# Optimization experiments

Hardware: AMD Instinct MI355X
Metric: run time of the kernel (lower is better)

The kernel has to match this reference:

```python
import jax, jax.numpy as jnp
from jax import lax
import numpy as np

B, GRID, H = 128, 28, 64      # batch, 28x28 pixel grid, hidden size
NDIR = 4                      # feature_sz = number of scan directions
FC_HD, OUT = 512, 10


def setup_inputs() -> dict:
    key = jax.random.key(0)
    ks = jax.random.split(key, 8)
    s_u = 1.0 / np.sqrt(2 * H)
    inp = {
        "x":  jax.random.normal(ks[0], (B, GRID, GRID), dtype=jnp.float32),
        # per-direction MDLSTM gate params: 5 gates (i, f_left, f_up, o, g)
        "Wx": jax.random.normal(ks[1], (NDIR, 5 * H), dtype=jnp.float32) * 0.1,
        "U":  jax.random.normal(ks[2], (NDIR, 2 * H, 5 * H), dtype=jnp.float32) * s_u,
        "b":  jnp.zeros((NDIR, 5 * H), dtype=jnp.float32),
        # fc head
        "W1": jax.random.normal(ks[3], (NDIR * H, FC_HD), dtype=jnp.float32) / np.sqrt(NDIR * H),
        "b1": jnp.zeros((FC_HD,), dtype=jnp.float32),
        "W2": jax.random.normal(ks[4], (FC_HD, OUT), dtype=jnp.float32) / np.sqrt(FC_HD),
        "b2": jnp.zeros((OUT,), dtype=jnp.float32),
    }
    return inp


def _mdlstm_dir(xg, Wx, U, b):
    # xg: [GRID(rows), GRID(cols), B] scalar pixel per cell
    zeros = jnp.zeros((xg.shape[-1], H), dtype=xg.dtype)

    def col_step(carry, inp):
        h_left, c_left = carry
        x_pix, h_up, c_up = inp                     # [B], [B,H], [B,H]
        z = x_pix[:, None] * Wx + jnp.concatenate([h_left, h_up], -1) @ U + b
        i, f1, f2, o, g = jnp.split(z, 5, axis=-1)  # each [B,H]
        c = (jax.nn.sigmoid(i) * jnp.tanh(g)
             + jax.nn.sigmoid(f1) * c_left
             + jax.nn.sigmoid(f2) * c_up)
        h = jax.nn.sigmoid(o) * jnp.tanh(c)
        return (h, c), (h, c)

    def row_step(carry, x_row):
        h_up_row, c_up_row = carry                  # [GRID,B,H] previous row
        _, (h_row, c_row) = lax.scan(col_step, (zeros, zeros),
                                     (x_row, h_up_row, c_up_row))
        return (h_row, c_row), None

    init = (jnp.zeros((GRID,) + zeros.shape, xg.dtype),
            jnp.zeros((GRID,) + zeros.shape, xg.dtype))
    (h_last_row, _), _ = lax.scan(row_step, init, xg)
    return h_last_row[-1]                           # final (bottom-right) hidden [B,H]


def _forward(x, Wx, U, b, W1, b1, W2, b2):
    x2 = x.reshape(-1, GRID, GRID)
    # 4 scan directions via flips; scan always proceeds top-left -> bottom-right
    dirs = jnp.stack([x2,
                      x2[:, :, ::-1],
                      x2[:, ::-1, :],
                      x2[:, ::-1, ::-1]], 0)        # [4,B,GRID,GRID]
    dirs = jnp.transpose(dirs, (0, 2, 3, 1))        # [4,GRID,GRID,B]
    h = jax.vmap(_mdlstm_dir)(dirs, Wx, U, b)       # [4,B,H]
    h = jnp.transpose(h, (1, 0, 2)).reshape(-1, NDIR * H)
    z = jax.nn.relu(h @ W1 + b1)
    return jax.nn.softmax(z @ W2 + b2, axis=-1)


def reference(x, Wx, U, b, W1, b1, W2, b2):
    return _forward(x, Wx, U, b, W1, b1, W2, b2)
```

## Files before the change

kernel.cpp:

```cpp
#include <hip/hip_runtime.h>
#include <hip/hip_bf16.h>


#define GRIDN 28
#define BATCH 128
#define HID   64
#define NDIR  4
#define FC_HD 512
#define OUT_N 10
#define BT    2
#define NSLOT 29
#define S_H   104
#define S_C   68

typedef _Float16 f16;
typedef _Float16 f16x8 __attribute__((ext_vector_type(8)));
typedef float    f32x4 __attribute__((ext_vector_type(4)));

__device__ __forceinline__ float sigf(float x) {
    return __builtin_amdgcn_rcpf(1.0f + __expf(-x));
}
__device__ __forceinline__ float tanh_fast(float x) {
    return 1.0f - 2.0f * __builtin_amdgcn_rcpf(1.0f + __expf(2.0f * x));
}

__global__ __launch_bounds__(512)
void mdlstm_kernel(const float* __restrict__ x,
                   const float* __restrict__ Wx,
                   const float* __restrict__ U,
                   const float* __restrict__ bias,
                   float* __restrict__ Hout)
{
    const int d    = blockIdx.x & 3;
    const int tile = blockIdx.x >> 2;
    const int tid  = threadIdx.x;
    const int lane = tid & 63;
    const int wave = tid >> 6;
    const int wm   = wave >> 2;
    const int wh   = wave & 3;
    const int l16  = lane & 15;
    const int q    = lane >> 4;
    const int nb   = wh * 16 + l16;

    __shared__ __align__(16) f16 Fh[2][BT][NSLOT * S_H];
    __shared__ float             Fc[2][BT][NSLOT * S_C];
    __shared__ float             xs[GRIDN][GRIDN][BT];

    for (int i = tid; i < 2 * BT * NSLOT * S_H; i += 512) ((f16*)Fh)[i] = (f16)0.0f;
    for (int i = tid; i < 2 * BT * NSLOT * S_C; i += 512) ((float*)Fc)[i] = 0.0f;
    for (int i = tid; i < GRIDN * GRIDN * BT; i += 512) {
        int bl = i & 1, rc = i >> 1, c = rc % GRIDN, r = rc / GRIDN;
        int rr = (d & 2) ? (GRIDN - 1 - r) : r;
        int cc = (d & 1) ? (GRIDN - 1 - c) : c;
        xs[r][c][bl] = x[((tile * BT + bl) * GRIDN + rr) * GRIDN + cc];
    }

    f16x8 bf[5][5];
#pragma unroll
    for (int g = 0; g < 5; ++g) {
        int n = g * 64 + nb;
#pragma unroll
        for (int ks = 0; ks < 4; ++ks) {
            f16x8 v;
            int kb = ks * 32 + q * 8;
#pragma unroll
            for (int j = 0; j < 8; ++j)
                v[j] = (f16)U[(d * 128 + kb + j) * 320 + n];
            bf[g][ks] = v;
        }
        f16x8 v5 = {(f16)0, (f16)0, (f16)0, (f16)0, (f16)0, (f16)0, (f16)0, (f16)0};
        if (q == 0) {
            v5[0] = (f16)Wx[d * 320 + n];
            v5[1] = (f16)bias[d * 320 + n];
        }
        bf[g][4] = v5;
    }
    __syncthreads();

    if (tid < 2 * BT * NSLOT) {
        int buf = tid / (BT * NSLOT), rem = tid % (BT * NSLOT);
        int b = rem / NSLOT, sl = rem % NSLOT;
        Fh[buf][b][sl * S_H + 65] = (f16)1.0f;
    }
    if (tid < BT) Fh[0][tid][27 * S_H + 64] = (f16)xs[0][0][tid];
    __syncthreads();

    for (int t = 0; t < 2 * GRIDN - 1; ++t) {
        const int rlo = (t > GRIDN - 1) ? (t - (GRIDN - 1)) : 0;
        const int rhi = (t < GRIDN - 1) ? t : (GRIDN - 1);
        const int k   = rhi - rlo + 1;
        const int nM  = (2 * k + 15) >> 4;
        const int br  = t & 1, bw = br ^ 1;

        if (t < 2 * GRIDN - 2 && tid >= 456) {
            int idx = tid - 456, b = idx & 1, j = idx >> 1;
            int rlo2 = (t + 1 > GRIDN - 1) ? (t + 1 - (GRIDN - 1)) : 0;
            int rhi2 = (t + 1 < GRIDN - 1) ? (t + 1) : (GRIDN - 1);
            if (j <= rhi2 - rlo2) {
                int r = rlo2 + j;
                Fh[bw][b][(27 - r) * S_H + 64] = (f16)xs[r][t + 1 - r][b];
            }
        }

        for (int mt = wm; mt < nM; mt += 2) {
            int mA = mt * 16 + l16;
            int jA = mA >> 1; if (jA > k - 1) jA = k - 1;
            int bA = mA & 1;
            int slA = 27 - (rlo + jA);
            const f16* ab = &Fh[br][bA][slA * S_H];
            f16x8 a0 = *(const f16x8*)(ab + q * 8);
            f16x8 a1 = *(const f16x8*)(ab + 32 + q * 8);
            f16x8 a2 = *(const f16x8*)(ab + S_H + q * 8);
            f16x8 a3 = *(const f16x8*)(ab + S_H + 32 + q * 8);
            f16x8 a4 = *(const f16x8*)(ab + 64 + q * 8);

            f32x4 acc[5];
#pragma unroll
            for (int g = 0; g < 5; ++g) acc[g] = (f32x4){0.f, 0.f, 0.f, 0.f};
#pragma unroll
            for (int g = 0; g < 5; ++g) acc[g] = __builtin_amdgcn_mfma_f32_16x16x32_f16(a0, bf[g][0], acc[g], 0, 0, 0);
#pragma unroll
            for (int g = 0; g < 5; ++g) acc[g] = __builtin_amdgcn_mfma_f32_16x16x32_f16(a1, bf[g][1], acc[g], 0, 0, 0);
#pragma unroll
            for (int g = 0; g < 5; ++g) acc[g] = __builtin_amdgcn_mfma_f32_16x16x32_f16(a2, bf[g][2], acc[g], 0, 0, 0);
#pragma unroll
            for (int g = 0; g < 5; ++g) acc[g] = __builtin_amdgcn_mfma_f32_16x16x32_f16(a3, bf[g][3], acc[g], 0, 0, 0);
#pragma unroll
            for (int g = 0; g < 5; ++g) acc[g] = __builtin_amdgcn_mfma_f32_16x16x32_f16(a4, bf[g][4], acc[g], 0, 0, 0);

            int j0  = mt * 8 + q * 2;
            int jj0 = (j0     > k - 1) ? k - 1 : j0;
            int jj1 = (j0 + 1 > k - 1) ? k - 1 : j0 + 1;
            int sl0 = 27 - (rlo + jj0);
            int sl1 = 27 - (rlo + jj1);
#pragma unroll
            for (int i = 0; i < 4; ++i) {
                int  b  = i & 1;
                int  sl = (i < 2) ? sl0 : sl1;
                float cl = Fc[br][b][sl * S_C + nb];
                float cu = Fc[br][b][(sl + 1) * S_C + nb];
                float ig = sigf(acc[0][i]);
                float f1 = sigf(acc[1][i]);
                float f2 = sigf(acc[2][i]);
                float og = sigf(acc[3][i]);
                float gg = tanh_fast(acc[4][i]);
                float cn = ig * gg + f1 * cl + f2 * cu;
                float hn = og * tanh_fast(cn);
                Fc[bw][b][sl * S_C + nb] = cn;
                Fh[bw][b][sl * S_H + nb] = (f16)hn;
            }
        }
        __syncthreads();
    }

    if (tid < BT * HID) {
        int bl = tid >> 6, h = tid & 63;
        Hout[(d * BATCH + tile * BT + bl) * HID + h] = (float)Fh[1][bl][h];
    }
}

__global__ __launch_bounds__(256)
void fc_kernel(const float* __restrict__ Hin,
               const float* __restrict__ W1, const float* __restrict__ b1,
               const float* __restrict__ W2, const float* __restrict__ b2,
               float* __restrict__ out)
{
    const int b   = blockIdx.x;
    const int tid = threadIdx.x;
    __shared__ float hrow[NDIR * HID];
    __shared__ float z1[FC_HD];
    __shared__ float ps[16][16];
    __shared__ float z2[16];

    hrow[tid] = Hin[(tid >> 6) * (BATCH * HID) + b * HID + (tid & 63)];
    __syncthreads();

    {
        float s0 = b1[tid], s1 = b1[tid + 256];
#pragma unroll 8
        for (int f = 0; f < NDIR * HID; ++f) {
            float h = hrow[f];
            s0 += h * W1[f * FC_HD + tid];
            s1 += h * W1[f * FC_HD + tid + 256];
        }
        z1[tid]       = fmaxf(s0, 0.0f);
        z1[tid + 256] = fmaxf(s1, 0.0f);
    }
    __syncthreads();

    {
        int j = tid & 15, sl = tid >> 4;
        float s = 0.0f;
        if (j < OUT_N) {
#pragma unroll
            for (int i = 0; i < 32; ++i) {
                int kk = sl * 32 + i;
                s += z1[kk] * W2[kk * OUT_N + j];
            }
        }
        ps[sl][j] = s;
    }
    __syncthreads();

    if (tid < OUT_N) {
        float s = b2[tid];
#pragma unroll
        for (int sl = 0; sl < 16; ++sl) s += ps[sl][tid];
        z2[tid] = s;
    }
    __syncthreads();

    if (tid == 0) {
        float m = z2[0];
        for (int j = 1; j < OUT_N; ++j) m = fmaxf(m, z2[j]);
        float sum = 0.0f, e[OUT_N];
        for (int j = 0; j < OUT_N; ++j) { e[j] = __expf(z2[j] - m); sum += e[j]; }
        float inv = 1.0f / sum;
        for (int j = 0; j < OUT_N; ++j) out[b * OUT_N + j] = e[j] * inv;
    }
}

extern "C" void kernel_launch(void* const* d_in, const int* in_sizes, int n_in,
                              void* d_out, int out_size, void* d_ws, size_t ws_size,
                              hipStream_t stream) {
    const float* x  = (const float*)d_in[0];
    const float* Wx = (const float*)d_in[1];
    const float* U  = (const float*)d_in[2];
    const float* bs = (const float*)d_in[3];
    const float* W1 = (const float*)d_in[4];
    const float* b1 = (const float*)d_in[5];
    const float* W2 = (const float*)d_in[6];
    const float* b2 = (const float*)d_in[7];
    float* out = (float*)d_out;
    float* Hws = (float*)d_ws;

    mdlstm_kernel<<<NDIR * (BATCH / BT), 512, 0, stream>>>(x, Wx, U, bs, Hws);
    fc_kernel<<<BATCH, 256, 0, stream>>>(Hws, W1, b1, W2, b2, out);
}
```

Baseline: 161.7 us.

## Process one batch element per block with 256 threads instead of two

Each MDLSTM block now handles a single batch sample with 4 waves instead of two samples with 8 waves, doubling the grid to 512 blocks. The diagonal wavefront rows map directly to MFMA M rows without interleaving batch, so the M-tile count per step halves per block. This raises block count and parallelism across CUs and lowers per-block shared memory, at the cost of MFMA tiles being less full (k cells per 16 rows) and more redundant weight loading and setup per block.

```diff
diff --git a/kernel.cpp b/kernel.cpp
--- a/kernel.cpp
+++ b/kernel.cpp
@@ -8,7 +8,6 @@
 #define NDIR  4
 #define FC_HD 512
 #define OUT_N 10
-#define BT    2
 #define NSLOT 29
 #define S_H   104
 #define S_C   68
@@ -24,7 +23,7 @@
     return 1.0f - 2.0f * __builtin_amdgcn_rcpf(1.0f + __expf(2.0f * x));
 }
 
-__global__ __launch_bounds__(512)
+__global__ __launch_bounds__(256)
 void mdlstm_kernel(const float* __restrict__ x,
                    const float* __restrict__ Wx,
                    const float* __restrict__ U,
@@ -32,27 +31,25 @@
                    float* __restrict__ Hout)
 {
     const int d    = blockIdx.x & 3;
-    const int tile = blockIdx.x >> 2;
+    const int bseq = blockIdx.x >> 2;
     const int tid  = threadIdx.x;
     const int lane = tid & 63;
-    const int wave = tid >> 6;
-    const int wm   = wave >> 2;
-    const int wh   = wave & 3;
+    const int wh   = tid >> 6;
     const int l16  = lane & 15;
     const int q    = lane >> 4;
     const int nb   = wh * 16 + l16;
 
-    __shared__ __align__(16) f16 Fh[2][BT][NSLOT * S_H];
-    __shared__ float             Fc[2][BT][NSLOT * S_C];
-    __shared__ float             xs[GRIDN][GRIDN][BT];
-
-    for (int i = tid; i < 2 * BT * NSLOT * S_H; i += 512) ((f16*)Fh)[i] = (f16)0.0f;
-    for (int i = tid; i < 2 * BT * NSLOT * S_C; i += 512) ((float*)Fc)[i] = 0.0f;
-    for (int i = tid; i < GRIDN * GRIDN * BT; i += 512) {
-        int bl = i & 1, rc = i >> 1, c = rc % GRIDN, r = rc / GRIDN;
+    __shared__ __align__(16) f16 Fh[2][NSLOT * S_H];
+    __shared__ float             Fc[2][NSLOT * S_C];
+    __shared__ float             xs[GRIDN][GRIDN];
+
+    for (int i = tid; i < 2 * NSLOT * S_H; i += 256) ((f16*)Fh)[i] = (f16)0.0f;
+    for (int i = tid; i < 2 * NSLOT * S_C; i += 256) ((float*)Fc)[i] = 0.0f;
+    for (int i = tid; i < GRIDN * GRIDN; i += 256) {
+        int c = i % GRIDN, r = i / GRIDN;
         int rr = (d & 2) ? (GRIDN - 1 - r) : r;
         int cc = (d & 1) ? (GRIDN - 1 - c) : c;
-        xs[r][c][bl] = x[((tile * BT + bl) * GRIDN + rr) * GRIDN + cc];
+        xs[r][c] = x[(bseq * GRIDN + rr) * GRIDN + cc];
     }
 
     f16x8 bf[5][5];
@@ -77,37 +74,35 @@
     }
     __syncthreads();
 
-    if (tid < 2 * BT * NSLOT) {
-        int buf = tid / (BT * NSLOT), rem = tid % (BT * NSLOT);
-        int b = rem / NSLOT, sl = rem % NSLOT;
-        Fh[buf][b][sl * S_H + 65] = (f16)1.0f;
-    }
-    if (tid < BT) Fh[0][tid][27 * S_H + 64] = (f16)xs[0][0][tid];
+    if (tid < 2 * NSLOT) {
+        int buf = tid / NSLOT, sl = tid % NSLOT;
+        Fh[buf][sl * S_H + 65] = (f16)1.0f;
+    }
+    if (tid == 0) Fh[0][27 * S_H + 64] = (f16)xs[0][0];
     __syncthreads();
 
     for (int t = 0; t < 2 * GRIDN - 1; ++t) {
         const int rlo = (t > GRIDN - 1) ? (t - (GRIDN - 1)) : 0;
         const int rhi = (t < GRIDN - 1) ? t : (GRIDN - 1);
         const int k   = rhi - rlo + 1;
-        const int nM  = (2 * k + 15) >> 4;
+        const int nM  = (k + 15) >> 4;
         const int br  = t & 1, bw = br ^ 1;
 
-        if (t < 2 * GRIDN - 2 && tid >= 456) {
-            int idx = tid - 456, b = idx & 1, j = idx >> 1;
+        if (t < 2 * GRIDN - 2 && tid >= 228) {
+            int j = tid - 228;
             int rlo2 = (t + 1 > GRIDN - 1) ? (t + 1 - (GRIDN - 1)) : 0;
             int rhi2 = (t + 1 < GRIDN - 1) ? (t + 1) : (GRIDN - 1);
             if (j <= rhi2 - rlo2) {
                 int r = rlo2 + j;
-                Fh[bw][b][(27 - r) * S_H + 64] = (f16)xs[r][t + 1 - r][b];
+                Fh[bw][(27 - r) * S_H + 64] = (f16)xs[r][t + 1 - r];
             }
         }
 
-        for (int mt = wm; mt < nM; mt += 2) {
+        for (int mt = 0; mt < nM; ++mt) {
             int mA = mt * 16 + l16;
-            int jA = mA >> 1; if (jA > k - 1) jA = k - 1;
-            int bA = mA & 1;
+            int jA = (mA > k - 1) ? k - 1 : mA;
             int slA = 27 - (rlo + jA);
-            const f16* ab = &Fh[br][bA][slA * S_H];
+            const f16* ab = &Fh[br][slA * S_H];
             f16x8 a0 = *(const f16x8*)(ab + q * 8);
             f16x8 a1 = *(const f16x8*)(ab + 32 + q * 8);
             f16x8 a2 = *(const f16x8*)(ab + S_H + q * 8);
@@ -128,17 +123,13 @@
 #pragma unroll
             for (int g = 0; g < 5; ++g) acc[g] = __builtin_amdgcn_mfma_f32_16x16x32_f16(a4, bf[g][4], acc[g], 0, 0, 0);
 
-            int j0  = mt * 8 + q * 2;
-            int jj0 = (j0     > k - 1) ? k - 1 : j0;
-            int jj1 = (j0 + 1 > k - 1) ? k - 1 : j0 + 1;
-            int sl0 = 27 - (rlo + jj0);
-            int sl1 = 27 - (rlo + jj1);
 #pragma unroll
             for (int i = 0; i < 4; ++i) {
-                int  b  = i & 1;
-                int  sl = (i < 2) ? sl0 : sl1;
-                float cl = Fc[br][b][sl * S_C + nb];
-                float cu = Fc[br][b][(sl + 1) * S_C + nb];
+                int rd = mt * 16 + q * 4 + i;
+                int jj = (rd > k - 1) ? k - 1 : rd;
+                int sl = 27 - (rlo + jj);
+                float cl = Fc[br][sl * S_C + nb];
+                float cu = Fc[br][(sl + 1) * S_C + nb];
                 float ig = sigf(acc[0][i]);
                 float f1 = sigf(acc[1][i]);
                 float f2 = sigf(acc[2][i]);
@@ -146,17 +137,15 @@
                 float gg = tanh_fast(acc[4][i]);
                 float cn = ig * gg + f1 * cl + f2 * cu;
                 float hn = og * tanh_fast(cn);
-                Fc[bw][b][sl * S_C + nb] = cn;
-                Fh[bw][b][sl * S_H + nb] = (f16)hn;
+                Fc[bw][sl * S_C + nb] = cn;
+                Fh[bw][sl * S_H + nb] = (f16)hn;
             }
         }
         __syncthreads();
     }
 
-    if (tid < BT * HID) {
-        int bl = tid >> 6, h = tid & 63;
-        Hout[(d * BATCH + tile * BT + bl) * HID + h] = (float)Fh[1][bl][h];
-    }
+    if (tid < HID)
+        Hout[(d * BATCH + bseq) * HID + tid] = (float)Fh[1][tid];
 }
 
 __global__ __launch_bounds__(256)
@@ -234,6 +223,6 @@
     float* out = (float*)d_out;
     float* Hws = (float*)d_ws;
 
-    mdlstm_kernel<<<NDIR * (BATCH / BT), 512, 0, stream>>>(x, Wx, U, bs, Hws);
+    mdlstm_kernel<<<NDIR * BATCH, 256, 0, stream>>>(x, Wx, U, bs, Hws);
     fc_kernel<<<BATCH, 256, 0, stream>>>(Hws, W1, b1, W2, b2, out);
 }
```

Measured after the change: 184.1 us. 13.8% more time.
